# Optimization experiments

Measured on AMD Instinct MI355X. Metric: run time of the kernel, lower is better.

Reference implementation:

```python
import jax, jax.numpy as jnp
import numpy as np

B, T, D, H = 2, 2048, 1024, 16
DH = D // H


def setup_inputs() -> dict:
    key = jax.random.key(0)
    k1, k2, k3, k4 = jax.random.split(key, 4)
    x = jax.random.normal(k1, (B, T, D), dtype=jnp.float32)
    k = jax.random.normal(k2, (B, H, T, DH), dtype=jnp.float32)
    v = jax.random.normal(k3, (B, H, T, DH), dtype=jnp.float32)
    Wq = jax.random.normal(k4, (D, D), dtype=jnp.float32) * (1.0 / np.sqrt(D))
    return {"x": x, "k": k, "v": v, "Wq": Wq}


def reference(x, k, v, Wq):
    b, t, d = x.shape
    h = k.shape[1]
    scale = 1.0 / jnp.sqrt(jnp.float32(d))  # note: sqrt(d), NOT sqrt(d/h), per source
    # q = Linear(d, d, bias=False): y = x @ Wq.T, then split into heads
    q = jnp.einsum('btd,ed->bte', x, Wq).reshape(b, t, h, -1).transpose(0, 2, 1, 3)  # [b,h,t,dh]
    scores = jnp.einsum('bhqd,bhkd->bhqk', q, k) * scale  # [b,h,t,t]
    causal = jnp.triu(jnp.ones((t, t), dtype=bool), k=1)  # True above diagonal -> masked
    scores = jnp.where(causal[None, None], -jnp.inf, scores)
    a = jax.nn.softmax(scores, axis=-1)
    out = jnp.einsum('bhqk,bhkd->bhqd', a, v).transpose(0, 2, 1, 3).reshape(b, t, d)
    return x + out
```

## Files before the change

kernel.cpp:

```cpp
#include <hip/hip_runtime.h>
#include <hip/hip_bf16.h>

#define B_ 2
#define T_ 2048
#define D_ 1024
#define H_ 16
#define DH_ 64

typedef __attribute__((ext_vector_type(8))) short bf16x8;
typedef __attribute__((ext_vector_type(4))) short bf16x4;
typedef __attribute__((ext_vector_type(4))) float f32x4;
typedef __attribute__((ext_vector_type(8))) unsigned short u16x8;

__device__ __forceinline__ unsigned short f2bf(float f) {
    unsigned int u = __float_as_uint(f);
    return (unsigned short)((u + 0x7FFFu + ((u >> 16) & 1u)) >> 16);
}

__device__ __forceinline__ void pack8(const float4& a, const float4& b, u16x8& o) {
    o[0] = f2bf(a.x); o[1] = f2bf(a.y); o[2] = f2bf(a.z); o[3] = f2bf(a.w);
    o[4] = f2bf(b.x); o[5] = f2bf(b.y); o[6] = f2bf(b.z); o[7] = f2bf(b.w);
}

__device__ __forceinline__ f32x4 mfma16(bf16x4 a, bf16x4 b, f32x4 c) {
#if defined(__HIP_DEVICE_COMPILE__)
    return __builtin_amdgcn_mfma_f32_16x16x16bf16_1k(a, b, c, 0, 0, 0);
#else
    return c;
#endif
}

__global__ __launch_bounds__(256) void fused_prep_qproj(
    const float* __restrict__ k, const float* __restrict__ v,
    const float* __restrict__ x, const float* __restrict__ Wq,
    unsigned short* __restrict__ kb, unsigned short* __restrict__ vt,
    unsigned short* __restrict__ qb)
{
    __shared__ __align__(16) char lds_raw[18432];
    const int tid = threadIdx.x;
    const int bi = blockIdx.x;

    if (bi >= 1024 && bi < 1536) {
        const int idx = bi - 1024;
        const float* src = k + ((size_t)idx * 256 + tid) * 32;
        unsigned short* dst = kb + ((size_t)idx * 256 + tid) * 32;
        #pragma unroll
        for (int u = 0; u < 4; ++u) {
            const float4 a = *(const float4*)(src + u * 8);
            const float4 b = *(const float4*)(src + u * 8 + 4);
            u16x8 o; pack8(a, b, o);
            *(u16x8*)(dst + u * 8) = o;
        }
        return;
    }

    if (bi >= 1536) {
        float (*Ts)[65] = (float(*)[65])lds_raw;
        const int idx = bi - 1536;
        const int t0 = (idx & 31) * 64;
        const int hb = idx >> 5;
        const size_t bh = (size_t)(hb >> 4) * H_ + (hb & 15);
        #pragma unroll
        for (int u = 0; u < 4; ++u) {
            const int tr = u * 16 + (tid >> 4);
            const int dc = (tid & 15) * 4;
            const float4 r = *(const float4*)(v + (bh * T_ + t0 + tr) * DH_ + dc);
            Ts[tr][dc + 0] = r.x; Ts[tr][dc + 1] = r.y;
            Ts[tr][dc + 2] = r.z; Ts[tr][dc + 3] = r.w;
        }
        __syncthreads();
        #pragma unroll
        for (int u = 0; u < 4; ++u) {
            const int dh = u * 16 + (tid >> 4);
            const int tc = (tid & 15) * 4;
            ushort4 o;
            o.x = f2bf(Ts[tc + 0][dh]); o.y = f2bf(Ts[tc + 1][dh]);
            o.z = f2bf(Ts[tc + 2][dh]); o.w = f2bf(Ts[tc + 3][dh]);
            *(ushort4*)(vt + (bh * DH_ + dh) * T_ + t0 + tc) = o;
        }
        return;
    }

    unsigned short (*As)[72] = (unsigned short(*)[72])lds_raw;
    unsigned short (*Bs)[72] = (unsigned short(*)[72])(lds_raw + 9216);

    const int m0 = (bi >> 4) * 64;
    const int h  = bi & 15;
    const int n0 = h * 64;

    const int lane = tid & 63;
    const int w = tid >> 6;
    const int l15 = lane & 15, l4 = lane >> 4;
    const int row = tid >> 2;
    const int c   = (tid & 3) * 16;

    f32x4 acc[4] = {};

    for (int k0 = 0; k0 < D_; k0 += 64) {
        {
            const float* g = x + (size_t)(m0 + row) * D_ + k0 + c;
            u16x8 p0, p1;
            pack8(*(const float4*)(g), *(const float4*)(g + 4), p0);
            pack8(*(const float4*)(g + 8), *(const float4*)(g + 12), p1);
            *(u16x8*)&As[row][c] = p0;
            *(u16x8*)&As[row][c + 8] = p1;
        }
        {
            const float* g = Wq + (size_t)(n0 + row) * D_ + k0 + c;
            u16x8 p0, p1;
            pack8(*(const float4*)(g), *(const float4*)(g + 4), p0);
            pack8(*(const float4*)(g + 8), *(const float4*)(g + 12), p1);
            *(u16x8*)&Bs[row][c] = p0;
            *(u16x8*)&Bs[row][c + 8] = p1;
        }
        __syncthreads();

        #pragma unroll
        for (int kc = 0; kc < 2; ++kc) {
            const bf16x8 af = *(const bf16x8*)&As[w * 16 + l15][kc * 32 + l4 * 8];
            #pragma unroll
            for (int nt = 0; nt < 4; ++nt) {
                const bf16x8 bfr = *(const bf16x8*)&Bs[nt * 16 + l15][kc * 32 + l4 * 8];
                acc[nt] = __builtin_amdgcn_mfma_f32_16x16x32_bf16(af, bfr, acc[nt], 0, 0, 0);
            }
        }
        __syncthreads();
    }

    const float scale = 1.0f / 32.0f;
    #pragma unroll
    for (int nt = 0; nt < 4; ++nt) {
        const int dh = nt * 16 + l15;
        #pragma unroll
        for (int r = 0; r < 4; ++r) {
            const int m = m0 + w * 16 + l4 * 4 + r;
            const int b = m >> 11, t = m & 2047;
            qb[(((size_t)b * H_ + h) * T_ + t) * DH_ + dh] = f2bf(acc[nt][r] * scale);
        }
    }
}

__global__ __launch_bounds__(256, 4) void attn_kernel(
    const unsigned short* __restrict__ qb,
    const unsigned short* __restrict__ kb,
    const unsigned short* __restrict__ vt,
    const float* __restrict__ xg,
    float* __restrict__ out)
{
    __shared__ unsigned short Ks[2][64][72];
    __shared__ unsigned short Vs[2][64][72];

    const int tid = threadIdx.x;
    const int lane = tid & 63;
    const int w = tid >> 6;
    const int l15 = lane & 15, l4 = lane >> 4;
    const int bi = blockIdx.x;
    const int qt = 31 - (bi >> 5);
    const int hb = bi & 31;
    const int h = hb & 15, b = hb >> 4;
    const int q0 = qt * 64;
    const size_t bh = (size_t)b * H_ + h;

    bf16x8 qf[2];
    #pragma unroll
    for (int kc = 0; kc < 2; ++kc)
        qf[kc] = *(const bf16x8*)(qb + (bh * T_ + q0 + w * 16 + l15) * DH_ + kc * 32 + l4 * 8);

    f32x4 o_acc[4] = {};
    float m_i = -INFINITY, l_i = 0.0f;

    const int srow = tid >> 2;
    const int scol = (tid & 3) * 16;

    {
        const unsigned short* gk = kb + (bh * T_ + srow) * DH_ + scol;
        *(uint4*)&Ks[0][srow][scol] = *(const uint4*)gk;
        *(uint4*)&Ks[0][srow][scol + 8] = *(const uint4*)(gk + 8);
        const unsigned short* gv = vt + (bh * DH_ + srow) * T_ + scol;
        *(uint4*)&Vs[0][srow][scol] = *(const uint4*)gv;
        *(uint4*)&Vs[0][srow][scol + 8] = *(const uint4*)(gv + 8);
    }
    __syncthreads();

    int p = 0;
    for (int j0 = 0; j0 <= q0; j0 += 64) {
        const int jn = (j0 + 64 <= q0) ? j0 + 64 : 0;
        uint4 kr0, kr1, vr0, vr1;
        {
            const unsigned short* gk = kb + (bh * T_ + jn + srow) * DH_ + scol;
            kr0 = *(const uint4*)gk;
            kr1 = *(const uint4*)(gk + 8);
            const unsigned short* gv = vt + (bh * DH_ + srow) * T_ + jn + scol;
            vr0 = *(const uint4*)gv;
            vr1 = *(const uint4*)(gv + 8);
        }

        f32x4 st[4] = {};
        #pragma unroll
        for (int kc = 0; kc < 2; ++kc) {
            #pragma unroll
            for (int nt = 0; nt < 4; ++nt) {
                const bf16x8 kf = *(const bf16x8*)&Ks[p][nt * 16 + l15][kc * 32 + l4 * 8];
                st[nt] = __builtin_amdgcn_mfma_f32_16x16x32_bf16(kf, qf[kc], st[nt], 0, 0, 0);
            }
        }

        if (j0 == q0) {
            const int thr = w * 16 + l15 - l4 * 4;
            #pragma unroll
            for (int nt = 0; nt < 4; ++nt)
                #pragma unroll
                for (int r = 0; r < 4; ++r)
                    if (nt * 16 + r > thr) st[nt][r] = -INFINITY;
        }

        float rm = -INFINITY;
        #pragma unroll
        for (int nt = 0; nt < 4; ++nt)
            #pragma unroll
            for (int r = 0; r < 4; ++r) rm = fmaxf(rm, st[nt][r]);
        rm = fmaxf(rm, __shfl_xor(rm, 16));
        rm = fmaxf(rm, __shfl_xor(rm, 32));
        const float mn = fmaxf(m_i, rm);
        const float alpha = __expf(m_i - mn);
        float rs = 0.0f;
        #pragma unroll
        for (int nt = 0; nt < 4; ++nt)
            #pragma unroll
            for (int r = 0; r < 4; ++r) {
                const float pv = __expf(st[nt][r] - mn);
                st[nt][r] = pv;
                rs += pv;
            }
        rs += __shfl_xor(rs, 16);
        rs += __shfl_xor(rs, 32);
        l_i = l_i * alpha + rs;
        m_i = mn;
        #pragma unroll
        for (int mt = 0; mt < 4; ++mt)
            #pragma unroll
            for (int r = 0; r < 4; ++r) o_acc[mt][r] *= alpha;

        bf16x4 pf[4];
        #pragma unroll
        for (int nt = 0; nt < 4; ++nt) {
            union { unsigned int u[2]; bf16x4 s; } cv;
            cv.u[0] = __builtin_amdgcn_perm(__float_as_uint(st[nt][1]),
                                            __float_as_uint(st[nt][0]), 0x07060302u);
            cv.u[1] = __builtin_amdgcn_perm(__float_as_uint(st[nt][3]),
                                            __float_as_uint(st[nt][2]), 0x07060302u);
            pf[nt] = cv.s;
        }

        #pragma unroll
        for (int c = 0; c < 4; ++c) {
            #pragma unroll
            for (int mt = 0; mt < 4; ++mt) {
                const bf16x4 vf = *(const bf16x4*)&Vs[p][mt * 16 + l15][c * 16 + l4 * 4];
                o_acc[mt] = mfma16(vf, pf[c], o_acc[mt]);
            }
        }

        *(uint4*)&Ks[p ^ 1][srow][scol] = kr0;
        *(uint4*)&Ks[p ^ 1][srow][scol + 8] = kr1;
        *(uint4*)&Vs[p ^ 1][srow][scol] = vr0;
        *(uint4*)&Vs[p ^ 1][srow][scol + 8] = vr1;
        __syncthreads();
        p ^= 1;
    }

    const float inv = 1.0f / l_i;
    const int qrow = q0 + w * 16 + l15;
    #pragma unroll
    for (int mt = 0; mt < 4; ++mt) {
        #pragma unroll
        for (int r = 0; r < 4; ++r) {
            const int d = h * DH_ + mt * 16 + l4 * 4 + r;
            const size_t off = ((size_t)b * T_ + qrow) * D_ + d;
            out[off] = xg[off] + o_acc[mt][r] * inv;
        }
    }
}

extern "C" void kernel_launch(void* const* d_in, const int* in_sizes, int n_in,
                              void* d_out, int out_size, void* d_ws, size_t ws_size,
                              hipStream_t stream) {
    const float* x  = (const float*)d_in[0];
    const float* k  = (const float*)d_in[1];
    const float* v  = (const float*)d_in[2];
    const float* Wq = (const float*)d_in[3];
    float* out = (float*)d_out;

    const size_t NE = (size_t)B_ * H_ * T_ * DH_;
    unsigned short* kb = (unsigned short*)d_ws;
    unsigned short* vt = kb + NE;
    unsigned short* qb = vt + NE;

    fused_prep_qproj<<<2560, 256, 0, stream>>>(k, v, x, Wq, kb, vt, qb);
    attn_kernel<<<1024, 256, 0, stream>>>(qb, kb, vt, x, out);
}
```

Before: 172.3 us.

## Fuse Q projection into attention kernel and switch softmax to exp2

The prep kernel now only converts k, x and Wq to bf16 and transposes v. The Q = x·Wqᵀ projection moves into the attention kernel: each block computes its 64×64 Q tile with MFMA, reading bf16 operands straight from global memory, and stages the result in LDS space that aliases the second K buffer. The log2(e) factor is folded into the Q scale so the softmax can use exp2f, and the LDS row padding drops from 72 to 68. This removes the separate Q GEMM pass and the qb round trip through memory. In exchange every attention block repeats an untiled 1024-deep reduction using strided global loads, which is extra front-loaded latency per block.

Result: slower. 279.3 us (+62.1%).

```diff
diff --git a/kernel.cpp b/kernel.cpp
--- a/kernel.cpp
+++ b/kernel.cpp
@@ -30,35 +30,19 @@
 #endif
 }
 
-__global__ __launch_bounds__(256) void fused_prep_qproj(
+__global__ __launch_bounds__(256) void conv_kernel(
     const float* __restrict__ k, const float* __restrict__ v,
     const float* __restrict__ x, const float* __restrict__ Wq,
     unsigned short* __restrict__ kb, unsigned short* __restrict__ vt,
-    unsigned short* __restrict__ qb)
+    unsigned short* __restrict__ xb, unsigned short* __restrict__ wqb)
 {
-    __shared__ __align__(16) char lds_raw[18432];
+    __shared__ float Ts[64][65];
     const int tid = threadIdx.x;
     const int bi = blockIdx.x;
 
-    if (bi >= 1024 && bi < 1536) {
-        const int idx = bi - 1024;
-        const float* src = k + ((size_t)idx * 256 + tid) * 32;
-        unsigned short* dst = kb + ((size_t)idx * 256 + tid) * 32;
-        #pragma unroll
-        for (int u = 0; u < 4; ++u) {
-            const float4 a = *(const float4*)(src + u * 8);
-            const float4 b = *(const float4*)(src + u * 8 + 4);
-            u16x8 o; pack8(a, b, o);
-            *(u16x8*)(dst + u * 8) = o;
-        }
-        return;
-    }
-
-    if (bi >= 1536) {
-        float (*Ts)[65] = (float(*)[65])lds_raw;
-        const int idx = bi - 1536;
-        const int t0 = (idx & 31) * 64;
-        const int hb = idx >> 5;
+    if (bi < 1024) {
+        const int t0 = (bi & 31) * 64;
+        const int hb = bi >> 5;
         const size_t bh = (size_t)(hb >> 4) * H_ + (hb & 15);
         #pragma unroll
         for (int u = 0; u < 4; ++u) {
@@ -81,74 +65,37 @@
         return;
     }
 
-    unsigned short (*As)[72] = (unsigned short(*)[72])lds_raw;
-    unsigned short (*Bs)[72] = (unsigned short(*)[72])(lds_raw + 9216);
-
-    const int m0 = (bi >> 4) * 64;
-    const int h  = bi & 15;
-    const int n0 = h * 64;
-
-    const int lane = tid & 63;
-    const int w = tid >> 6;
-    const int l15 = lane & 15, l4 = lane >> 4;
-    const int row = tid >> 2;
-    const int c   = (tid & 3) * 16;
-
-    f32x4 acc[4] = {};
-
-    for (int k0 = 0; k0 < D_; k0 += 64) {
-        {
-            const float* g = x + (size_t)(m0 + row) * D_ + k0 + c;
-            u16x8 p0, p1;
-            pack8(*(const float4*)(g), *(const float4*)(g + 4), p0);
-            pack8(*(const float4*)(g + 8), *(const float4*)(g + 12), p1);
-            *(u16x8*)&As[row][c] = p0;
-            *(u16x8*)&As[row][c + 8] = p1;
-        }
-        {
-            const float* g = Wq + (size_t)(n0 + row) * D_ + k0 + c;
-            u16x8 p0, p1;
-            pack8(*(const float4*)(g), *(const float4*)(g + 4), p0);
-            pack8(*(const float4*)(g + 8), *(const float4*)(g + 12), p1);
-            *(u16x8*)&Bs[row][c] = p0;
-            *(u16x8*)&Bs[row][c + 8] = p1;
-        }
-        __syncthreads();
-
-        #pragma unroll
-        for (int kc = 0; kc < 2; ++kc) {
-            const bf16x8 af = *(const bf16x8*)&As[w * 16 + l15][kc * 32 + l4 * 8];
-            #pragma unroll
-            for (int nt = 0; nt < 4; ++nt) {
-                const bf16x8 bfr = *(const bf16x8*)&Bs[nt * 16 + l15][kc * 32 + l4 * 8];
-                acc[nt] = __builtin_amdgcn_mfma_f32_16x16x32_bf16(af, bfr, acc[nt], 0, 0, 0);
-            }
-        }
-        __syncthreads();
-    }
-
-    const float scale = 1.0f / 32.0f;
+    const float* src;
+    unsigned short* dst;
+    if (bi < 1536)      { src = k  + ((size_t)(bi - 1024) * 256 + tid) * 32;
+                          dst = kb  + ((size_t)(bi - 1024) * 256 + tid) * 32; }
+    else if (bi < 2048) { src = x  + ((size_t)(bi - 1536) * 256 + tid) * 32;
+                          dst = xb  + ((size_t)(bi - 1536) * 256 + tid) * 32; }
+    else                { src = Wq + ((size_t)(bi - 2048) * 256 + tid) * 32;
+                          dst = wqb + ((size_t)(bi - 2048) * 256 + tid) * 32; }
     #pragma unroll
-    for (int nt = 0; nt < 4; ++nt) {
-        const int dh = nt * 16 + l15;
-        #pragma unroll
-        for (int r = 0; r < 4; ++r) {
-            const int m = m0 + w * 16 + l4 * 4 + r;
-            const int b = m >> 11, t = m & 2047;
-            qb[(((size_t)b * H_ + h) * T_ + t) * DH_ + dh] = f2bf(acc[nt][r] * scale);
-        }
+    for (int u = 0; u < 4; ++u) {
+        const float4 a = *(const float4*)(src + u * 8);
+        const float4 b = *(const float4*)(src + u * 8 + 4);
+        u16x8 o; pack8(a, b, o);
+        *(u16x8*)(dst + u * 8) = o;
     }
 }
 
 __global__ __launch_bounds__(256, 4) void attn_kernel(
-    const unsigned short* __restrict__ qb,
+    const unsigned short* __restrict__ xb,
+    const unsigned short* __restrict__ wqb,
     const unsigned short* __restrict__ kb,
     const unsigned short* __restrict__ vt,
     const float* __restrict__ xg,
     float* __restrict__ out)
 {
-    __shared__ unsigned short Ks[2][64][72];
-    __shared__ unsigned short Vs[2][64][72];
+    __shared__ __align__(16) char lds_raw[34816];
+    unsigned short (*Ks0)[68] = (unsigned short(*)[68])(lds_raw);
+    unsigned short (*Vs0)[68] = (unsigned short(*)[68])(lds_raw + 8704);
+    unsigned short (*Ks1)[68] = (unsigned short(*)[68])(lds_raw + 17408);
+    unsigned short (*Vs1)[68] = (unsigned short(*)[68])(lds_raw + 26112);
+    unsigned short (*Qs)[68]  = (unsigned short(*)[68])(lds_raw + 17408);
 
     const int tid = threadIdx.x;
     const int lane = tid & 63;
@@ -161,10 +108,32 @@
     const int q0 = qt * 64;
     const size_t bh = (size_t)b * H_ + h;
 
+    {
+        f32x4 acc[4] = {};
+        const unsigned short* xr  = xb  + ((size_t)b * T_ + q0 + w * 16 + l15) * D_ + l4 * 8;
+        const unsigned short* wr0 = wqb + (size_t)(h * 64 + l15) * D_ + l4 * 8;
+        #pragma unroll 4
+        for (int kk = 0; kk < D_; kk += 32) {
+            const bf16x8 xf = *(const bf16x8*)(xr + kk);
+            #pragma unroll
+            for (int mt = 0; mt < 4; ++mt) {
+                const bf16x8 wf = *(const bf16x8*)(wr0 + (size_t)(mt * 16) * D_ + kk);
+                acc[mt] = __builtin_amdgcn_mfma_f32_16x16x32_bf16(wf, xf, acc[mt], 0, 0, 0);
+            }
+        }
+        const float qscale = 1.4426950408889634f / 32.0f;
+        #pragma unroll
+        for (int mt = 0; mt < 4; ++mt) {
+            ushort4 o;
+            o.x = f2bf(acc[mt][0] * qscale); o.y = f2bf(acc[mt][1] * qscale);
+            o.z = f2bf(acc[mt][2] * qscale); o.w = f2bf(acc[mt][3] * qscale);
+            *(ushort4*)&Qs[w * 16 + l15][mt * 16 + l4 * 4] = o;
+        }
+    }
     bf16x8 qf[2];
     #pragma unroll
     for (int kc = 0; kc < 2; ++kc)
-        qf[kc] = *(const bf16x8*)(qb + (bh * T_ + q0 + w * 16 + l15) * DH_ + kc * 32 + l4 * 8);
+        qf[kc] = *(const bf16x8*)&Qs[w * 16 + l15][kc * 32 + l4 * 8];
 
     f32x4 o_acc[4] = {};
     float m_i = -INFINITY, l_i = 0.0f;
@@ -174,16 +143,21 @@
 
     {
         const unsigned short* gk = kb + (bh * T_ + srow) * DH_ + scol;
-        *(uint4*)&Ks[0][srow][scol] = *(const uint4*)gk;
-        *(uint4*)&Ks[0][srow][scol + 8] = *(const uint4*)(gk + 8);
+        *(uint4*)&Ks0[srow][scol] = *(const uint4*)gk;
+        *(uint4*)&Ks0[srow][scol + 8] = *(const uint4*)(gk + 8);
         const unsigned short* gv = vt + (bh * DH_ + srow) * T_ + scol;
-        *(uint4*)&Vs[0][srow][scol] = *(const uint4*)gv;
-        *(uint4*)&Vs[0][srow][scol + 8] = *(const uint4*)(gv + 8);
+        *(uint4*)&Vs0[srow][scol] = *(const uint4*)gv;
+        *(uint4*)&Vs0[srow][scol + 8] = *(const uint4*)(gv + 8);
     }
     __syncthreads();
 
     int p = 0;
     for (int j0 = 0; j0 <= q0; j0 += 64) {
+        unsigned short (*Ksp)[68] = p ? Ks1 : Ks0;
+        unsigned short (*Vsp)[68] = p ? Vs1 : Vs0;
+        unsigned short (*Ksn)[68] = p ? Ks0 : Ks1;
+        unsigned short (*Vsn)[68] = p ? Vs0 : Vs1;
+
         const int jn = (j0 + 64 <= q0) ? j0 + 64 : 0;
         uint4 kr0, kr1, vr0, vr1;
         {
@@ -200,7 +174,7 @@
         for (int kc = 0; kc < 2; ++kc) {
             #pragma unroll
             for (int nt = 0; nt < 4; ++nt) {
-                const bf16x8 kf = *(const bf16x8*)&Ks[p][nt * 16 + l15][kc * 32 + l4 * 8];
+                const bf16x8 kf = *(const bf16x8*)&Ksp[nt * 16 + l15][kc * 32 + l4 * 8];
                 st[nt] = __builtin_amdgcn_mfma_f32_16x16x32_bf16(kf, qf[kc], st[nt], 0, 0, 0);
             }
         }
@@ -222,13 +196,13 @@
         rm = fmaxf(rm, __shfl_xor(rm, 16));
         rm = fmaxf(rm, __shfl_xor(rm, 32));
         const float mn = fmaxf(m_i, rm);
-        const float alpha = __expf(m_i - mn);
+        const float alpha = exp2f(m_i - mn);
         float rs = 0.0f;
         #pragma unroll
         for (int nt = 0; nt < 4; ++nt)
             #pragma unroll
             for (int r = 0; r < 4; ++r) {
-                const float pv = __expf(st[nt][r] - mn);
+                const float pv = exp2f(st[nt][r] - mn);
                 st[nt][r] = pv;
                 rs += pv;
             }
@@ -256,15 +230,15 @@
         for (int c = 0; c < 4; ++c) {
             #pragma unroll
             for (int mt = 0; mt < 4; ++mt) {
-                const bf16x4 vf = *(const bf16x4*)&Vs[p][mt * 16 + l15][c * 16 + l4 * 4];
+                const bf16x4 vf = *(const bf16x4*)&Vsp[mt * 16 + l15][c * 16 + l4 * 4];
                 o_acc[mt] = mfma16(vf, pf[c], o_acc[mt]);
             }
         }
 
-        *(uint4*)&Ks[p ^ 1][srow][scol] = kr0;
-        *(uint4*)&Ks[p ^ 1][srow][scol + 8] = kr1;
-        *(uint4*)&Vs[p ^ 1][srow][scol] = vr0;
-        *(uint4*)&Vs[p ^ 1][srow][scol + 8] = vr1;
+        *(uint4*)&Ksn[srow][scol] = kr0;
+        *(uint4*)&Ksn[srow][scol + 8] = kr1;
+        *(uint4*)&Vsn[srow][scol] = vr0;
+        *(uint4*)&Vsn[srow][scol + 8] = vr1;
         __syncthreads();
         p ^= 1;
     }
@@ -292,10 +266,11 @@
     float* out = (float*)d_out;
 
     const size_t NE = (size_t)B_ * H_ * T_ * DH_;
-    unsigned short* kb = (unsigned short*)d_ws;
-    unsigned short* vt = kb + NE;
-    unsigned short* qb = vt + NE;
-
-    fused_prep_qproj<<<2560, 256, 0, stream>>>(k, v, x, Wq, kb, vt, qb);
-    attn_kernel<<<1024, 256, 0, stream>>>(qb, kb, vt, x, out);
-}
+    unsigned short* kb  = (unsigned short*)d_ws;
+    unsigned short* vt  = kb + NE;
+    unsigned short* xb  = vt + NE;
+    unsigned short* wqb = xb + NE;
+
+    conv_kernel<<<2176, 256, 0, stream>>>(k, v, x, Wq, kb, vt, xb, wqb);
+    attn_kernel<<<1024, 256, 0, stream>>>(xb, wqb, kb, vt, x, out);
+}
```
